# Optimization experiments

Hardware: AMD Instinct MI355X
Metric: run time of the kernel (lower is better)

## Reference

```python
import jax, jax.numpy as jnp
import numpy as np

N_NODES = 50000
N_EDGES = 600000
IN_DIM = 128
HID = 128
FEAT = 128
N_TASKS = 5
N_CLS = 10


def setup_inputs() -> dict:
    key = jax.random.key(0)
    ks = jax.random.split(key, 10)
    s = 0.05  # small init scale for weights
    return {
        "x": jax.random.normal(ks[0], (N_NODES, IN_DIM), jnp.float32),
        "edge_index": jax.random.randint(ks[1], (2, N_EDGES), 0, N_NODES, dtype=jnp.int32),
        "w1": jax.random.normal(ks[2], (IN_DIM, HID), jnp.float32) * s,
        "b1": jnp.zeros((HID,), jnp.float32),
        "w2": jax.random.normal(ks[3], (HID, HID), jnp.float32) * s,
        "b2": jnp.zeros((HID,), jnp.float32),
        "fw1": jax.random.normal(ks[4], (HID, FEAT), jnp.float32) * s,
        "fb1": jnp.zeros((FEAT,), jnp.float32),
        "fw2": jax.random.normal(ks[5], (FEAT, FEAT), jnp.float32) * s,
        "fb2": jnp.zeros((FEAT,), jnp.float32),
        "task_w": jax.random.normal(ks[6], (N_TASKS, FEAT, N_CLS), jnp.float32) * s,
        "task_b": jnp.zeros((N_TASKS, N_CLS), jnp.float32),
    }


def reference(x, edge_index, w1, b1, w2, b2, fw1, fb1, fw2, fb2, task_w, task_b):
    n = x.shape[0]
    # PyG GCNConv: add self-loops, symmetric D^{-1/2} A D^{-1/2} normalization.
    loop = jnp.arange(n, dtype=edge_index.dtype)
    src = jnp.concatenate([edge_index[0], loop])  # source nodes
    dst = jnp.concatenate([edge_index[1], loop])  # target (aggregation) nodes
    deg = jnp.zeros((n,), x.dtype).at[dst].add(jnp.ones((), x.dtype))
    dinv = jnp.where(deg > 0, jax.lax.rsqrt(deg), 0.0)
    norm = dinv[src] * dinv[dst]  # [E+N]

    def gcn_conv(h, w, b):
        h = h @ w                         # [N, H] linear transform
        msg = h[src] * norm[:, None]      # gather + normalize  [E+N, H]
        agg = jnp.zeros((n, h.shape[1]), h.dtype).at[dst].add(msg)  # scatter-add
        return agg + b

    h = jax.nn.relu(gcn_conv(x, w1, b1))
    # dropout(0.5) is identity at inference
    h = jax.nn.relu(gcn_conv(h, w2, b2))
    feature_x = jax.nn.relu(h @ fw1 + fb1)   # fc1
    h2 = jax.nn.relu(feature_x @ fw2 + fb2)  # fc2
    # per-task heads, all 128->10: batched as one einsum  [T, N, C]
    y = jnp.einsum('nf,tfc->tnc', h2, task_w) + task_b[:, None, :]
    return (y, feature_x)
```

## Files before the change

kernel.cpp:

```cpp
#include <hip/hip_runtime.h>
#include <hip/hip_bf16.h>

#define NN 50000
#define NE 600000
#define MM1_BLOCKS 1564
#define STRIDE 64

typedef __attribute__((ext_vector_type(4))) float f32x4;
typedef __attribute__((ext_vector_type(8))) __bf16 bf16x8;

__device__ __forceinline__ unsigned pack2bf16(float x, float y) {
  __bf16 lo = (__bf16)x, hi = (__bf16)y;
  unsigned short ul = __builtin_bit_cast(unsigned short, lo);
  unsigned short uh = __builtin_bit_cast(unsigned short, hi);
  return (unsigned)ul | ((unsigned)uh << 16);
}

__global__ void k_zero(int* __restrict__ degi) {
  int i = blockIdx.x * 256 + threadIdx.x;
  if (i < NN) degi[i] = 0;
}

__global__ void k_prep(const int* __restrict__ degi, int* __restrict__ cur,
                       float* __restrict__ dinv, int2* __restrict__ edg) {
  int n = blockIdx.x * 256 + threadIdx.x;
  if (n < NN) {
    int d = degi[n];
    int base = n * STRIDE;
    cur[n] = base;
    dinv[n] = rsqrtf((float)(d + 1));
    int pe = base + ((d + 7) & ~7);
    for (int j = base + d; j < pe; j++) edg[j] = make_int2(0, 0);
  }
}

__global__ void k_fill(const int* __restrict__ srcv, const int* __restrict__ dstv,
                       int* __restrict__ cur, int2* __restrict__ edg, const float* __restrict__ dinv) {
  int e = blockIdx.x * 256 + threadIdx.x;
  if (e < NE) {
    int s = srcv[e], d = dstv[e];
    int p = atomicAdd(&cur[d], 1);
    edg[p] = make_int2(s, __float_as_int(dinv[s] * dinv[d]));
  }
}

__device__ __forceinline__ void stage_wt64(const float* __restrict__ W, __bf16 (*wt)[136],
                                           int tid, int colbase) {
  int j = tid & 63;
  int kh = tid >> 6;
#pragma unroll
  for (int it = 0; it < 16; ++it) {
    int kp = ((it << 2) + kh + (j >> 3)) & 63;
    float w0 = W[(kp * 2) * 128 + colbase + j];
    float w1 = W[(kp * 2 + 1) * 128 + colbase + j];
    *(unsigned*)(&wt[j][kp * 2]) = pack2bf16(w0, w1);
  }
}

template<int BR, bool IN_BF16, bool DUAL>
__device__ __forceinline__ void mm_body64(const void* __restrict__ Xv, const __bf16 (*wt)[136],
                                          const float* __restrict__ bias, __bf16* __restrict__ Y,
                                          float* __restrict__ Yf, int strip, int lane, int colbase) {
  int r16 = lane & 15, g = lane >> 4;
  bf16x8 a[4];
  if constexpr (IN_BF16) {
    const __bf16* xb = (const __bf16*)Xv + (size_t)(strip * 16 + r16) * 128 + g * 8;
#pragma unroll
    for (int ks = 0; ks < 4; ks++) a[ks] = *(const bf16x8*)(xb + ks * 32);
  } else {
    const float* xb = (const float*)Xv + (size_t)(strip * 16 + r16) * 128 + g * 8;
#pragma unroll
    for (int ks = 0; ks < 4; ks++) {
      f32x4 x0 = *(const f32x4*)(xb + ks * 32);
      f32x4 x1 = *(const f32x4*)(xb + ks * 32 + 4);
      bf16x8 v;
      v[0] = (__bf16)x0.x; v[1] = (__bf16)x0.y; v[2] = (__bf16)x0.z; v[3] = (__bf16)x0.w;
      v[4] = (__bf16)x1.x; v[5] = (__bf16)x1.y; v[6] = (__bf16)x1.z; v[7] = (__bf16)x1.w;
      a[ks] = v;
    }
  }
  f32x4 acc[4];
#pragma unroll
  for (int ct = 0; ct < 4; ct++) acc[ct] = (f32x4){0.f, 0.f, 0.f, 0.f};
#pragma unroll
  for (int ct = 0; ct < 4; ct++) {
    const __bf16* wrow = &wt[ct * 16 + r16][g * 8];
#pragma unroll
    for (int ks = 0; ks < 4; ks++) {
      bf16x8 b = *(const bf16x8*)(wrow + ks * 32);
      acc[ct] = __builtin_amdgcn_mfma_f32_16x16x32_bf16(a[ks], b, acc[ct], 0, 0, 0);
    }
  }
  int rbase = strip * 16 + g * 4;
#pragma unroll
  for (int ct = 0; ct < 4; ct++) {
    int col = colbase + ct * 16 + r16;
    float bv = (BR & 1) ? bias[col] : 0.f;
#pragma unroll
    for (int i = 0; i < 4; i++) {
      float v = acc[ct][i] + bv;
      if (BR & 2) v = fmaxf(v, 0.f);
      size_t idx = (size_t)(rbase + i) * 128 + col;
      Y[idx] = (__bf16)v;
      if constexpr (DUAL) Yf[idx] = v;
    }
  }
}

template<int BR, bool IN_BF16, bool DUAL>
__global__ __launch_bounds__(256) void k_mm64(const void* __restrict__ Xv, const float* __restrict__ W,
                                              const float* __restrict__ bias, __bf16* __restrict__ Y,
                                              float* __restrict__ Yf, int nrows) {
  __shared__ __bf16 wt[64][136];
  int tid = threadIdx.x;
  int colbase = (blockIdx.x & 1) << 6;
  stage_wt64(W, wt, tid, colbase);
  __syncthreads();
  int strip = (blockIdx.x >> 1) * 4 + (tid >> 6);
  if (strip * 16 >= nrows) return;
  mm_body64<BR, IN_BF16, DUAL>(Xv, wt, bias, Y, Yf, strip, tid & 63, colbase);
}

__global__ __launch_bounds__(256) void k_mm1_count(const float* __restrict__ X, const float* __restrict__ W,
                                                   __bf16* __restrict__ Y,
                                                   const int* __restrict__ dstv, int* __restrict__ degi) {
  __shared__ __bf16 wt[64][136];
  int tid = threadIdx.x;
  if (blockIdx.x >= MM1_BLOCKS) {
    int e = (blockIdx.x - MM1_BLOCKS) * 256 + tid;
    if (e < NE) atomicAdd(&degi[dstv[e]], 1);
    return;
  }
  int colbase = (blockIdx.x & 1) << 6;
  stage_wt64(W, wt, tid, colbase);
  __syncthreads();
  int strip = (blockIdx.x >> 1) * 4 + (tid >> 6);
  if (strip * 16 >= NN) return;
  mm_body64<0, false, false>(X, wt, nullptr, Y, nullptr, strip, tid & 63, colbase);
}

__global__ __launch_bounds__(256) void k_head(const __bf16* __restrict__ H, const float* __restrict__ TW,
                                              const float* __restrict__ TB, float* __restrict__ Y) {
  __shared__ __bf16 wt[64][136];
  int tid = threadIdx.x;
#pragma unroll
  for (int it = 0; it < 32; it++) {
    int i = it * 256 + tid;
    int o = i >> 7, k = i & 127;
    float v = (o < 50) ? TW[(o / 10) * 1280 + k * 10 + (o % 10)] : 0.f;
    wt[o][k] = (__bf16)v;
  }
  __syncthreads();
  int lane = tid & 63;
  int strip = blockIdx.x * 4 + (tid >> 6);
  if (strip * 16 >= NN) return;
  int r16 = lane & 15, g = lane >> 4;
  const __bf16* xb = H + (size_t)(strip * 16 + r16) * 128 + g * 8;
  bf16x8 a[4];
#pragma unroll
  for (int ks = 0; ks < 4; ks++) a[ks] = *(const bf16x8*)(xb + ks * 32);
  f32x4 acc[4];
#pragma unroll
  for (int ct = 0; ct < 4; ct++) acc[ct] = (f32x4){0.f, 0.f, 0.f, 0.f};
#pragma unroll
  for (int ct = 0; ct < 4; ct++) {
    const __bf16* wrow = &wt[ct * 16 + r16][g * 8];
#pragma unroll
    for (int ks = 0; ks < 4; ks++) {
      bf16x8 b = *(const bf16x8*)(wrow + ks * 32);
      acc[ct] = __builtin_amdgcn_mfma_f32_16x16x32_bf16(a[ks], b, acc[ct], 0, 0, 0);
    }
  }
  int rbase = strip * 16 + g * 4;
#pragma unroll
  for (int ct = 0; ct < 4; ct++) {
    int o = ct * 16 + r16;
    if (o < 50) {
      int t = o / 10, c = o % 10;
      float tb = TB[o];
#pragma unroll
      for (int i = 0; i < 4; i++) {
        Y[(size_t)t * (NN * 10) + (size_t)(rbase + i) * 10 + c] = acc[ct][i] + tb;
      }
    }
  }
}

__device__ __forceinline__ void edge8(const int2* __restrict__ edg, int i, const unsigned* __restrict__ T,
                                      int lane, float& ax, float& ay) {
  const int4* ep = (const int4*)(edg + i);
  int4 p0 = ep[0], p1 = ep[1], p2 = ep[2], p3 = ep[3];
  unsigned v0 = T[p0.x * 64 + lane];
  unsigned v1 = T[p0.z * 64 + lane];
  unsigned v2 = T[p1.x * 64 + lane];
  unsigned v3 = T[p1.z * 64 + lane];
  unsigned v4 = T[p2.x * 64 + lane];
  unsigned v5 = T[p2.z * 64 + lane];
  unsigned v6 = T[p3.x * 64 + lane];
  unsigned v7 = T[p3.z * 64 + lane];
  float w0 = __int_as_float(p0.y), w1 = __int_as_float(p0.w);
  float w2 = __int_as_float(p1.y), w3 = __int_as_float(p1.w);
  float w4 = __int_as_float(p2.y), w5 = __int_as_float(p2.w);
  float w6 = __int_as_float(p3.y), w7 = __int_as_float(p3.w);
  ax = fmaf(__uint_as_float(v0 << 16), w0, ax); ay = fmaf(__uint_as_float(v0 & 0xffff0000u), w0, ay);
  ax = fmaf(__uint_as_float(v1 << 16), w1, ax); ay = fmaf(__uint_as_float(v1 & 0xffff0000u), w1, ay);
  ax = fmaf(__uint_as_float(v2 << 16), w2, ax); ay = fmaf(__uint_as_float(v2 & 0xffff0000u), w2, ay);
  ax = fmaf(__uint_as_float(v3 << 16), w3, ax); ay = fmaf(__uint_as_float(v3 & 0xffff0000u), w3, ay);
  ax = fmaf(__uint_as_float(v4 << 16), w4, ax); ay = fmaf(__uint_as_float(v4 & 0xffff0000u), w4, ay);
  ax = fmaf(__uint_as_float(v5 << 16), w5, ax); ay = fmaf(__uint_as_float(v5 & 0xffff0000u), w5, ay);
  ax = fmaf(__uint_as_float(v6 << 16), w6, ax); ay = fmaf(__uint_as_float(v6 & 0xffff0000u), w6, ay);
  ax = fmaf(__uint_as_float(v7 << 16), w7, ax); ay = fmaf(__uint_as_float(v7 & 0xffff0000u), w7, ay);
}

__global__ __launch_bounds__(256) void k_agg(const unsigned* __restrict__ T, const int* __restrict__ degi,
                                             const int2* __restrict__ edg, const float* __restrict__ dinv,
                                             const float* __restrict__ bias, unsigned* __restrict__ H) {
  int pair = blockIdx.x * 4 + (threadIdx.x >> 6);
  int nA = pair * 2, nB = nA + 1;
  int lane = threadIdx.x & 63;
  float2 b = ((const float2*)bias)[lane];
  float diA = dinv[nA], diB = dinv[nB];
  unsigned tA = T[(size_t)nA * 64 + lane];
  unsigned tB = T[(size_t)nB * 64 + lane];
  float axA = __uint_as_float(tA << 16) * (diA * diA);
  float ayA = __uint_as_float(tA & 0xffff0000u) * (diA * diA);
  float axB = __uint_as_float(tB << 16) * (diB * diB);
  float ayB = __uint_as_float(tB & 0xffff0000u) * (diB * diB);
  int iA = nA * STRIDE, eA = iA + ((degi[nA] + 7) & ~7);
  int iB = nB * STRIDE, eB = iB + ((degi[nB] + 7) & ~7);
  while (iA < eA && iB < eB) {
    edge8(edg, iA, T, lane, axA, ayA);
    edge8(edg, iB, T, lane, axB, ayB);
    iA += 8; iB += 8;
  }
  for (; iA < eA; iA += 8) edge8(edg, iA, T, lane, axA, ayA);
  for (; iB < eB; iB += 8) edge8(edg, iB, T, lane, axB, ayB);
  H[(size_t)nA * 64 + lane] = pack2bf16(fmaxf(axA + b.x, 0.f), fmaxf(ayA + b.y, 0.f));
  H[(size_t)nB * 64 + lane] = pack2bf16(fmaxf(axB + b.x, 0.f), fmaxf(ayB + b.y, 0.f));
}

extern "C" void kernel_launch(void* const* d_in, const int* in_sizes, int n_in,
                              void* d_out, int out_size, void* d_ws, size_t ws_size,
                              hipStream_t stream) {
  (void)in_sizes; (void)n_in; (void)out_size; (void)ws_size;
  const float* x   = (const float*)d_in[0];
  const int*   ei  = (const int*)d_in[1];
  const float* w1  = (const float*)d_in[2];
  const float* b1  = (const float*)d_in[3];
  const float* w2  = (const float*)d_in[4];
  const float* b2  = (const float*)d_in[5];
  const float* fw1 = (const float*)d_in[6];
  const float* fb1 = (const float*)d_in[7];
  const float* fw2 = (const float*)d_in[8];
  const float* fb2 = (const float*)d_in[9];
  const float* tw  = (const float*)d_in[10];
  const float* tb  = (const float*)d_in[11];
  const int* srcv = ei;
  const int* dstv = ei + NE;

  char* wsb = (char*)d_ws;
  __bf16* bufT = (__bf16*)(wsb + 0);
  __bf16* hbf  = (__bf16*)(wsb + 12800000);
  int*    degi = (int*)(wsb + 25600000);
  int*    cur  = (int*)(wsb + 25800192);
  float*  dinv = (float*)(wsb + 26000640);
  int2*   edg  = (int2*)(wsb + 26201088);

  float* y_out = (float*)d_out;
  float* feat  = (float*)d_out + 2500000;

  k_zero<<<196, 256, 0, stream>>>(degi);
  k_mm1_count<<<MM1_BLOCKS + (NE + 255) / 256, 256, 0, stream>>>(x, w1, bufT, dstv, degi);
  k_prep<<<196, 256, 0, stream>>>(degi, cur, dinv, edg);
  k_fill<<<(NE + 255) / 256, 256, 0, stream>>>(srcv, dstv, cur, edg, dinv);

  k_agg<<<6250, 256, 0, stream>>>((const unsigned*)bufT, degi, edg, dinv, b1, (unsigned*)hbf);
  k_mm64<0, true, false><<<1564, 256, 0, stream>>>(hbf, w2, nullptr, bufT, nullptr, NN);
  k_agg<<<6250, 256, 0, stream>>>((const unsigned*)bufT, degi, edg, dinv, b2, (unsigned*)hbf);
  k_mm64<3, true, true><<<1564, 256, 0, stream>>>(hbf, fw1, fb1, bufT, feat, NN);
  k_mm64<3, true, false><<<1564, 256, 0, stream>>>(bufT, fw2, fb2, hbf, nullptr, NN);
  k_head<<<782, 256, 0, stream>>>(hbf, tw, tb, y_out);
}
```

Baseline: 176.0 us.

## Compress edge lists to 16-bit indices and fuse fill/prep kernels

```diff
diff --git a/kernel.cpp b/kernel.cpp
--- a/kernel.cpp
+++ b/kernel.cpp
@@ -4,6 +4,7 @@
 #define NN 50000
 #define NE 600000
 #define MM1_BLOCKS 1564
+#define FILL_BLOCKS 2344
 #define STRIDE 64
 
 typedef __attribute__((ext_vector_type(4))) float f32x4;
@@ -16,31 +17,35 @@
   return (unsigned)ul | ((unsigned)uh << 16);
 }
 
-__global__ void k_zero(int* __restrict__ degi) {
+__device__ __forceinline__ float lo16(unsigned v) { return __uint_as_float(v << 16); }
+__device__ __forceinline__ float hi16(unsigned v) { return __uint_as_float(v & 0xffff0000u); }
+
+__global__ void k_zero(int* __restrict__ degi, int* __restrict__ cur) {
   int i = blockIdx.x * 256 + threadIdx.x;
-  if (i < NN) degi[i] = 0;
-}
-
-__global__ void k_prep(const int* __restrict__ degi, int* __restrict__ cur,
-                       float* __restrict__ dinv, int2* __restrict__ edg) {
-  int n = blockIdx.x * 256 + threadIdx.x;
-  if (n < NN) {
-    int d = degi[n];
-    int base = n * STRIDE;
-    cur[n] = base;
-    dinv[n] = rsqrtf((float)(d + 1));
-    int pe = base + ((d + 7) & ~7);
-    for (int j = base + d; j < pe; j++) edg[j] = make_int2(0, 0);
-  }
-}
-
-__global__ void k_fill(const int* __restrict__ srcv, const int* __restrict__ dstv,
-                       int* __restrict__ cur, int2* __restrict__ edg, const float* __restrict__ dinv) {
-  int e = blockIdx.x * 256 + threadIdx.x;
-  if (e < NE) {
-    int s = srcv[e], d = dstv[e];
-    int p = atomicAdd(&cur[d], 1);
-    edg[p] = make_int2(s, __float_as_int(dinv[s] * dinv[d]));
+  if (i < NN) { degi[i] = 0; cur[i] = 0; }
+}
+
+__global__ void k_fillprep(const int* __restrict__ srcv, const int* __restrict__ dstv,
+                           const int* __restrict__ degi, int* __restrict__ cur,
+                           unsigned short* __restrict__ eds, float* __restrict__ dinv) {
+  int bid = blockIdx.x, tid = threadIdx.x;
+  if (bid < FILL_BLOCKS) {
+    int e = bid * 256 + tid;
+    if (e < NE) {
+      int s = srcv[e], d = dstv[e];
+      int p = d * STRIDE + atomicAdd(&cur[d], 1);
+      eds[p] = (unsigned short)s;
+    }
+  } else {
+    int n = (bid - FILL_BLOCKS) * 256 + tid;
+    if (n < NN) {
+      int d = degi[n];
+      dinv[n] = rsqrtf((float)(d + 1));
+      int base = n * STRIDE;
+      int pe = base + ((d + 7) & ~7);
+      for (int j = base + d; j < pe; j++) eds[j] = (unsigned short)NN;
+    }
+    if (n == NN) dinv[NN] = 0.f;
   }
 }
 
@@ -186,57 +191,57 @@
   }
 }
 
-__device__ __forceinline__ void edge8(const int2* __restrict__ edg, int i, const unsigned* __restrict__ T,
-                                      int lane, float& ax, float& ay) {
-  const int4* ep = (const int4*)(edg + i);
-  int4 p0 = ep[0], p1 = ep[1], p2 = ep[2], p3 = ep[3];
-  unsigned v0 = T[p0.x * 64 + lane];
-  unsigned v1 = T[p0.z * 64 + lane];
-  unsigned v2 = T[p1.x * 64 + lane];
-  unsigned v3 = T[p1.z * 64 + lane];
-  unsigned v4 = T[p2.x * 64 + lane];
-  unsigned v5 = T[p2.z * 64 + lane];
-  unsigned v6 = T[p3.x * 64 + lane];
-  unsigned v7 = T[p3.z * 64 + lane];
-  float w0 = __int_as_float(p0.y), w1 = __int_as_float(p0.w);
-  float w2 = __int_as_float(p1.y), w3 = __int_as_float(p1.w);
-  float w4 = __int_as_float(p2.y), w5 = __int_as_float(p2.w);
-  float w6 = __int_as_float(p3.y), w7 = __int_as_float(p3.w);
-  ax = fmaf(__uint_as_float(v0 << 16), w0, ax); ay = fmaf(__uint_as_float(v0 & 0xffff0000u), w0, ay);
-  ax = fmaf(__uint_as_float(v1 << 16), w1, ax); ay = fmaf(__uint_as_float(v1 & 0xffff0000u), w1, ay);
-  ax = fmaf(__uint_as_float(v2 << 16), w2, ax); ay = fmaf(__uint_as_float(v2 & 0xffff0000u), w2, ay);
-  ax = fmaf(__uint_as_float(v3 << 16), w3, ax); ay = fmaf(__uint_as_float(v3 & 0xffff0000u), w3, ay);
-  ax = fmaf(__uint_as_float(v4 << 16), w4, ax); ay = fmaf(__uint_as_float(v4 & 0xffff0000u), w4, ay);
-  ax = fmaf(__uint_as_float(v5 << 16), w5, ax); ay = fmaf(__uint_as_float(v5 & 0xffff0000u), w5, ay);
-  ax = fmaf(__uint_as_float(v6 << 16), w6, ax); ay = fmaf(__uint_as_float(v6 & 0xffff0000u), w6, ay);
-  ax = fmaf(__uint_as_float(v7 << 16), w7, ax); ay = fmaf(__uint_as_float(v7 & 0xffff0000u), w7, ay);
-}
-
 __global__ __launch_bounds__(256) void k_agg(const unsigned* __restrict__ T, const int* __restrict__ degi,
-                                             const int2* __restrict__ edg, const float* __restrict__ dinv,
+                                             const unsigned short* __restrict__ eds,
+                                             const float* __restrict__ dinv,
                                              const float* __restrict__ bias, unsigned* __restrict__ H) {
-  int pair = blockIdx.x * 4 + (threadIdx.x >> 6);
-  int nA = pair * 2, nB = nA + 1;
-  int lane = threadIdx.x & 63;
-  float2 b = ((const float2*)bias)[lane];
-  float diA = dinv[nA], diB = dinv[nB];
-  unsigned tA = T[(size_t)nA * 64 + lane];
-  unsigned tB = T[(size_t)nB * 64 + lane];
-  float axA = __uint_as_float(tA << 16) * (diA * diA);
-  float ayA = __uint_as_float(tA & 0xffff0000u) * (diA * diA);
-  float axB = __uint_as_float(tB << 16) * (diB * diB);
-  float ayB = __uint_as_float(tB & 0xffff0000u) * (diB * diB);
-  int iA = nA * STRIDE, eA = iA + ((degi[nA] + 7) & ~7);
-  int iB = nB * STRIDE, eB = iB + ((degi[nB] + 7) & ~7);
-  while (iA < eA && iB < eB) {
-    edge8(edg, iA, T, lane, axA, ayA);
-    edge8(edg, iB, T, lane, axB, ayB);
-    iA += 8; iB += 8;
-  }
-  for (; iA < eA; iA += 8) edge8(edg, iA, T, lane, axA, ayA);
-  for (; iB < eB; iB += 8) edge8(edg, iB, T, lane, axB, ayB);
-  H[(size_t)nA * 64 + lane] = pack2bf16(fmaxf(axA + b.x, 0.f), fmaxf(ayA + b.y, 0.f));
-  H[(size_t)nB * 64 + lane] = pack2bf16(fmaxf(axB + b.x, 0.f), fmaxf(ayB + b.y, 0.f));
+  int bid = blockIdx.x;
+  int q = (bid & 7) >> 1;
+  int nb = (bid >> 3) * 2 + (bid & 1);
+  if (nb >= 3125) return;
+  int tid = threadIdx.x;
+  int node = nb * 16 + (tid >> 4);
+  int off = (q << 4) + (tid & 15);
+  float dn = dinv[node];
+  int d = degi[node];
+  int e = (d + 7) & ~7;
+  const uint4* ed4 = (const uint4*)(eds + node * STRIDE);
+  float ax = 0.f, ay = 0.f;
+  for (int i = 0; i < e; i += 8) {
+    uint4 ev = ed4[i >> 3];
+    int s0 = ev.x & 0xffff, s1 = ev.x >> 16;
+    int s2 = ev.y & 0xffff, s3 = ev.y >> 16;
+    int s4 = ev.z & 0xffff, s5 = ev.z >> 16;
+    int s6 = ev.w & 0xffff, s7 = ev.w >> 16;
+    float w0 = dinv[s0], w1 = dinv[s1], w2 = dinv[s2], w3 = dinv[s3];
+    float w4 = dinv[s4], w5 = dinv[s5], w6 = dinv[s6], w7 = dinv[s7];
+    unsigned v0 = T[s0 * 64 + off];
+    unsigned v1 = T[s1 * 64 + off];
+    unsigned v2 = T[s2 * 64 + off];
+    unsigned v3 = T[s3 * 64 + off];
+    unsigned v4 = T[s4 * 64 + off];
+    unsigned v5 = T[s5 * 64 + off];
+    unsigned v6 = T[s6 * 64 + off];
+    unsigned v7 = T[s7 * 64 + off];
+    w0 *= dn; w1 *= dn; w2 *= dn; w3 *= dn;
+    w4 *= dn; w5 *= dn; w6 *= dn; w7 *= dn;
+    ax = fmaf(lo16(v0), w0, ax); ay = fmaf(hi16(v0), w0, ay);
+    ax = fmaf(lo16(v1), w1, ax); ay = fmaf(hi16(v1), w1, ay);
+    ax = fmaf(lo16(v2), w2, ax); ay = fmaf(hi16(v2), w2, ay);
+    ax = fmaf(lo16(v3), w3, ax); ay = fmaf(hi16(v3), w3, ay);
+    ax = fmaf(lo16(v4), w4, ax); ay = fmaf(hi16(v4), w4, ay);
+    ax = fmaf(lo16(v5), w5, ax); ay = fmaf(hi16(v5), w5, ay);
+    ax = fmaf(lo16(v6), w6, ax); ay = fmaf(hi16(v6), w6, ay);
+    ax = fmaf(lo16(v7), w7, ax); ay = fmaf(hi16(v7), w7, ay);
+  }
+  unsigned t0 = T[node * 64 + off];
+  float sl = dn * dn;
+  ax = fmaf(lo16(t0), sl, ax);
+  ay = fmaf(hi16(t0), sl, ay);
+  float2 bv = ((const float2*)bias)[off];
+  ax = fmaxf(ax + bv.x, 0.f);
+  ay = fmaxf(ay + bv.y, 0.f);
+  H[node * 64 + off] = pack2bf16(ax, ay);
 }
 
 extern "C" void kernel_launch(void* const* d_in, const int* in_sizes, int n_in,
@@ -262,21 +267,20 @@
   __bf16* bufT = (__bf16*)(wsb + 0);
   __bf16* hbf  = (__bf16*)(wsb + 12800000);
   int*    degi = (int*)(wsb + 25600000);
-  int*    cur  = (int*)(wsb + 25800192);
-  float*  dinv = (float*)(wsb + 26000640);
-  int2*   edg  = (int2*)(wsb + 26201088);
+  int*    cur  = (int*)(wsb + 25800000);
+  float*  dinv = (float*)(wsb + 26000000);
+  unsigned short* eds = (unsigned short*)(wsb + 26200064);
 
   float* y_out = (float*)d_out;
   float* feat  = (float*)d_out + 2500000;
 
-  k_zero<<<196, 256, 0, stream>>>(degi);
+  k_zero<<<196, 256, 0, stream>>>(degi, cur);
   k_mm1_count<<<MM1_BLOCKS + (NE + 255) / 256, 256, 0, stream>>>(x, w1, bufT, dstv, degi);
-  k_prep<<<196, 256, 0, stream>>>(degi, cur, dinv, edg);
-  k_fill<<<(NE + 255) / 256, 256, 0, stream>>>(srcv, dstv, cur, edg, dinv);
-
-  k_agg<<<6250, 256, 0, stream>>>((const unsigned*)bufT, degi, edg, dinv, b1, (unsigned*)hbf);
+  k_fillprep<<<FILL_BLOCKS + 196, 256, 0, stream>>>(srcv, dstv, degi, cur, eds, dinv);
+
+  k_agg<<<12512, 256, 0, stream>>>((const unsigned*)bufT, degi, eds, dinv, b1, (unsigned*)hbf);
   k_mm64<0, true, false><<<1564, 256, 0, stream>>>(hbf, w2, nullptr, bufT, nullptr, NN);
-  k_agg<<<6250, 256, 0, stream>>>((const unsigned*)bufT, degi, edg, dinv, b2, (unsigned*)hbf);
+  k_agg<<<12512, 256, 0, stream>>>((const unsigned*)bufT, degi, eds, dinv, b2, (unsigned*)hbf);
   k_mm64<3, true, true><<<1564, 256, 0, stream>>>(hbf, fw1, fb1, bufT, feat, NN);
   k_mm64<3, true, false><<<1564, 256, 0, stream>>>(bufT, fw2, fb2, hbf, nullptr, NN);
   k_head<<<782, 256, 0, stream>>>(hbf, tw, tb, y_out);
```

Result: slower. 202.5 us (+15.1%).

## Fuse CSR fill into mm1 kernel and compute edge norms on the fly

Applied to the files above, without the earlier changes.

```diff
diff --git a/kernel.cpp b/kernel.cpp
--- a/kernel.cpp
+++ b/kernel.cpp
@@ -4,6 +4,7 @@
 #define NN 50000
 #define NE 600000
 #define MM1_BLOCKS 1564
+#define FILL_BLOCKS 2344
 #define STRIDE 64
 
 typedef __attribute__((ext_vector_type(4))) float f32x4;
@@ -16,32 +17,26 @@
   return (unsigned)ul | ((unsigned)uh << 16);
 }
 
-__global__ void k_zero(int* __restrict__ degi) {
+__device__ __forceinline__ float lo16(unsigned v) { return __uint_as_float(v << 16); }
+__device__ __forceinline__ float hi16(unsigned v) { return __uint_as_float(v & 0xffff0000u); }
+
+__global__ void k_zero(int* __restrict__ cur) {
   int i = blockIdx.x * 256 + threadIdx.x;
-  if (i < NN) degi[i] = 0;
-}
-
-__global__ void k_prep(const int* __restrict__ degi, int* __restrict__ cur,
+  if (i < NN) cur[i] = 0;
+}
+
+__global__ void k_prep(const int* __restrict__ cur, int* __restrict__ degi,
                        float* __restrict__ dinv, int2* __restrict__ edg) {
   int n = blockIdx.x * 256 + threadIdx.x;
   if (n < NN) {
-    int d = degi[n];
+    int d = cur[n];
+    degi[n] = d;
+    dinv[n] = rsqrtf((float)(d + 1));
     int base = n * STRIDE;
-    cur[n] = base;
-    dinv[n] = rsqrtf((float)(d + 1));
     int pe = base + ((d + 7) & ~7);
-    for (int j = base + d; j < pe; j++) edg[j] = make_int2(0, 0);
-  }
-}
-
-__global__ void k_fill(const int* __restrict__ srcv, const int* __restrict__ dstv,
-                       int* __restrict__ cur, int2* __restrict__ edg, const float* __restrict__ dinv) {
-  int e = blockIdx.x * 256 + threadIdx.x;
-  if (e < NE) {
-    int s = srcv[e], d = dstv[e];
-    int p = atomicAdd(&cur[d], 1);
-    edg[p] = make_int2(s, __float_as_int(dinv[s] * dinv[d]));
-  }
+    for (int j = base + d; j < pe; j++) edg[j] = make_int2(NN, NN);
+  }
+  if (n == 0) dinv[NN] = 0.f;
 }
 
 __device__ __forceinline__ void stage_wt64(const float* __restrict__ W, __bf16 (*wt)[136],
@@ -121,14 +116,19 @@
   mm_body64<BR, IN_BF16, DUAL>(Xv, wt, bias, Y, Yf, strip, tid & 63, colbase);
 }
 
-__global__ __launch_bounds__(256) void k_mm1_count(const float* __restrict__ X, const float* __restrict__ W,
-                                                   __bf16* __restrict__ Y,
-                                                   const int* __restrict__ dstv, int* __restrict__ degi) {
+__global__ __launch_bounds__(256) void k_mm1_fill(const float* __restrict__ X, const float* __restrict__ W,
+                                                  __bf16* __restrict__ Y,
+                                                  const int* __restrict__ srcv, const int* __restrict__ dstv,
+                                                  int* __restrict__ cur, int2* __restrict__ edg) {
   __shared__ __bf16 wt[64][136];
   int tid = threadIdx.x;
   if (blockIdx.x >= MM1_BLOCKS) {
     int e = (blockIdx.x - MM1_BLOCKS) * 256 + tid;
-    if (e < NE) atomicAdd(&degi[dstv[e]], 1);
+    if (e < NE) {
+      int s = srcv[e], d = dstv[e];
+      int p = d * STRIDE + atomicAdd(&cur[d], 1);
+      edg[p] = make_int2(s, s);
+    }
     return;
   }
   int colbase = (blockIdx.x & 1) << 6;
@@ -187,29 +187,32 @@
 }
 
 __device__ __forceinline__ void edge8(const int2* __restrict__ edg, int i, const unsigned* __restrict__ T,
+                                      const float* __restrict__ dinv, float dn,
                                       int lane, float& ax, float& ay) {
   const int4* ep = (const int4*)(edg + i);
   int4 p0 = ep[0], p1 = ep[1], p2 = ep[2], p3 = ep[3];
-  unsigned v0 = T[p0.x * 64 + lane];
-  unsigned v1 = T[p0.z * 64 + lane];
-  unsigned v2 = T[p1.x * 64 + lane];
-  unsigned v3 = T[p1.z * 64 + lane];
-  unsigned v4 = T[p2.x * 64 + lane];
-  unsigned v5 = T[p2.z * 64 + lane];
-  unsigned v6 = T[p3.x * 64 + lane];
-  unsigned v7 = T[p3.z * 64 + lane];
-  float w0 = __int_as_float(p0.y), w1 = __int_as_float(p0.w);
-  float w2 = __int_as_float(p1.y), w3 = __int_as_float(p1.w);
-  float w4 = __int_as_float(p2.y), w5 = __int_as_float(p2.w);
-  float w6 = __int_as_float(p3.y), w7 = __int_as_float(p3.w);
-  ax = fmaf(__uint_as_float(v0 << 16), w0, ax); ay = fmaf(__uint_as_float(v0 & 0xffff0000u), w0, ay);
-  ax = fmaf(__uint_as_float(v1 << 16), w1, ax); ay = fmaf(__uint_as_float(v1 & 0xffff0000u), w1, ay);
-  ax = fmaf(__uint_as_float(v2 << 16), w2, ax); ay = fmaf(__uint_as_float(v2 & 0xffff0000u), w2, ay);
-  ax = fmaf(__uint_as_float(v3 << 16), w3, ax); ay = fmaf(__uint_as_float(v3 & 0xffff0000u), w3, ay);
-  ax = fmaf(__uint_as_float(v4 << 16), w4, ax); ay = fmaf(__uint_as_float(v4 & 0xffff0000u), w4, ay);
-  ax = fmaf(__uint_as_float(v5 << 16), w5, ax); ay = fmaf(__uint_as_float(v5 & 0xffff0000u), w5, ay);
-  ax = fmaf(__uint_as_float(v6 << 16), w6, ax); ay = fmaf(__uint_as_float(v6 & 0xffff0000u), w6, ay);
-  ax = fmaf(__uint_as_float(v7 << 16), w7, ax); ay = fmaf(__uint_as_float(v7 & 0xffff0000u), w7, ay);
+  int s0 = p0.x, s1 = p0.z, s2 = p1.x, s3 = p1.z;
+  int s4 = p2.x, s5 = p2.z, s6 = p3.x, s7 = p3.z;
+  float w0 = dinv[s0], w1 = dinv[s1], w2 = dinv[s2], w3 = dinv[s3];
+  float w4 = dinv[s4], w5 = dinv[s5], w6 = dinv[s6], w7 = dinv[s7];
+  unsigned v0 = T[s0 * 64 + lane];
+  unsigned v1 = T[s1 * 64 + lane];
+  unsigned v2 = T[s2 * 64 + lane];
+  unsigned v3 = T[s3 * 64 + lane];
+  unsigned v4 = T[s4 * 64 + lane];
+  unsigned v5 = T[s5 * 64 + lane];
+  unsigned v6 = T[s6 * 64 + lane];
+  unsigned v7 = T[s7 * 64 + lane];
+  w0 *= dn; w1 *= dn; w2 *= dn; w3 *= dn;
+  w4 *= dn; w5 *= dn; w6 *= dn; w7 *= dn;
+  ax = fmaf(lo16(v0), w0, ax); ay = fmaf(hi16(v0), w0, ay);
+  ax = fmaf(lo16(v1), w1, ax); ay = fmaf(hi16(v1), w1, ay);
+  ax = fmaf(lo16(v2), w2, ax); ay = fmaf(hi16(v2), w2, ay);
+  ax = fmaf(lo16(v3), w3, ax); ay = fmaf(hi16(v3), w3, ay);
+  ax = fmaf(lo16(v4), w4, ax); ay = fmaf(hi16(v4), w4, ay);
+  ax = fmaf(lo16(v5), w5, ax); ay = fmaf(hi16(v5), w5, ay);
+  ax = fmaf(lo16(v6), w6, ax); ay = fmaf(hi16(v6), w6, ay);
+  ax = fmaf(lo16(v7), w7, ax); ay = fmaf(hi16(v7), w7, ay);
 }
 
 __global__ __launch_bounds__(256) void k_agg(const unsigned* __restrict__ T, const int* __restrict__ degi,
@@ -222,19 +225,19 @@
   float diA = dinv[nA], diB = dinv[nB];
   unsigned tA = T[(size_t)nA * 64 + lane];
   unsigned tB = T[(size_t)nB * 64 + lane];
-  float axA = __uint_as_float(tA << 16) * (diA * diA);
-  float ayA = __uint_as_float(tA & 0xffff0000u) * (diA * diA);
-  float axB = __uint_as_float(tB << 16) * (diB * diB);
-  float ayB = __uint_as_float(tB & 0xffff0000u) * (diB * diB);
+  float axA = lo16(tA) * (diA * diA);
+  float ayA = hi16(tA) * (diA * diA);
+  float axB = lo16(tB) * (diB * diB);
+  float ayB = hi16(tB) * (diB * diB);
   int iA = nA * STRIDE, eA = iA + ((degi[nA] + 7) & ~7);
   int iB = nB * STRIDE, eB = iB + ((degi[nB] + 7) & ~7);
   while (iA < eA && iB < eB) {
-    edge8(edg, iA, T, lane, axA, ayA);
-    edge8(edg, iB, T, lane, axB, ayB);
+    edge8(edg, iA, T, dinv, diA, lane, axA, ayA);
+    edge8(edg, iB, T, dinv, diB, lane, axB, ayB);
     iA += 8; iB += 8;
   }
-  for (; iA < eA; iA += 8) edge8(edg, iA, T, lane, axA, ayA);
-  for (; iB < eB; iB += 8) edge8(edg, iB, T, lane, axB, ayB);
+  for (; iA < eA; iA += 8) edge8(edg, iA, T, dinv, diA, lane, axA, ayA);
+  for (; iB < eB; iB += 8) edge8(edg, iB, T, dinv, diB, lane, axB, ayB);
   H[(size_t)nA * 64 + lane] = pack2bf16(fmaxf(axA + b.x, 0.f), fmaxf(ayA + b.y, 0.f));
   H[(size_t)nB * 64 + lane] = pack2bf16(fmaxf(axB + b.x, 0.f), fmaxf(ayB + b.y, 0.f));
 }
@@ -262,17 +265,16 @@
   __bf16* bufT = (__bf16*)(wsb + 0);
   __bf16* hbf  = (__bf16*)(wsb + 12800000);
   int*    degi = (int*)(wsb + 25600000);
-  int*    cur  = (int*)(wsb + 25800192);
-  float*  dinv = (float*)(wsb + 26000640);
-  int2*   edg  = (int2*)(wsb + 26201088);
+  int*    cur  = (int*)(wsb + 25800000);
+  float*  dinv = (float*)(wsb + 26000000);
+  int2*   edg  = (int2*)(wsb + 26200064);
 
   float* y_out = (float*)d_out;
   float* feat  = (float*)d_out + 2500000;
 
-  k_zero<<<196, 256, 0, stream>>>(degi);
-  k_mm1_count<<<MM1_BLOCKS + (NE + 255) / 256, 256, 0, stream>>>(x, w1, bufT, dstv, degi);
-  k_prep<<<196, 256, 0, stream>>>(degi, cur, dinv, edg);
-  k_fill<<<(NE + 255) / 256, 256, 0, stream>>>(srcv, dstv, cur, edg, dinv);
+  k_zero<<<196, 256, 0, stream>>>(cur);
+  k_mm1_fill<<<MM1_BLOCKS + FILL_BLOCKS, 256, 0, stream>>>(x, w1, bufT, srcv, dstv, cur, edg);
+  k_prep<<<196, 256, 0, stream>>>(cur, degi, dinv, edg);
 
   k_agg<<<6250, 256, 0, stream>>>((const unsigned*)bufT, degi, edg, dinv, b1, (unsigned*)hbf);
   k_mm64<0, true, false><<<1564, 256, 0, stream>>>(hbf, w2, nullptr, bufT, nullptr, NN);
```

Result: faster. 153.2 us, median of 2 (-12.9%).
